# Optimization experiments

Measured on AMD Instinct MI355X. Metric: run time of the kernel, lower is better.

## Reference

```python
import jax, jax.numpy as jnp
import numpy as np

N_NODES = 100000
N_RADIAL = 16  # columns 0..15
N_CONICAL = 16  # columns 16..31


def setup_inputs() -> dict:
    key = jax.random.key(0)
    k1, k2, k3, k4 = jax.random.split(key, 4)
    x = jax.random.normal(k1, (N_NODES, 32), dtype=jnp.float32)
    edge_index = jax.random.randint(k2, (2, 1600000), 0, N_NODES, dtype=jnp.int32)
    W1 = jax.random.normal(k3, (32, 128), dtype=jnp.float32) * 0.1
    b1 = jnp.zeros((128,), dtype=jnp.float32)
    W2 = jax.random.normal(k4, (128, 32), dtype=jnp.float32) * 0.1
    b2 = jnp.zeros((32,), dtype=jnp.float32)
    return {"x": x, "edge_index": edge_index, "W1": W1, "b1": b1, "W2": W2, "b2": b2}


def reference(x, edge_index, W1, b1, W2, b2):
    # slice radial / conical feature channels
    radial = x[:, :N_RADIAL]            # [N, 16]
    conical = x[:, N_RADIAL:N_RADIAL + N_CONICAL]  # [N, 16]

    i, j = edge_index[0], edge_index[1]
    rows = jnp.concatenate([i, j])      # symmetrized COO rows [2E]
    cols = jnp.concatenate([j, i])      # symmetrized COO cols [2E]

    # coalesce()+sparse.mm == segment-sum over all (duplicated) entries
    neighbor_sum = jax.ops.segment_sum(conical[cols], rows, num_segments=N_NODES)  # [N, 16]
    deg = jax.ops.segment_sum(jnp.ones_like(rows, dtype=x.dtype), rows, num_segments=N_NODES)
    deg = jnp.clip(deg, 1.0)[:, None]   # bincount(...).clamp(min=1)
    agg = neighbor_sum / deg            # mean aggregation

    combined = jnp.concatenate([radial, agg], axis=1)  # [N, 32]
    h = jax.nn.relu(combined @ W1 + b1)
    out = h @ W2 + b2                   # [N, 32]
    return out
```

## Files before the change

kernel.cpp:

```cpp
#include <hip/hip_runtime.h>
#include <hip/hip_fp16.h>

#define N_NODES  100000
#define N_RADIAL 16
#define N_CONICAL 16

#define NPB    256
#define NBKT   ((N_NODES + NPB - 1) / NPB)
#define NBLK_A 500
#define BTHR   512
#define CHUNK  6400
#define BINSTRIDE 6400
#define CAP    10240

typedef _Float16 h2vec __attribute__((ext_vector_type(2)));
static __device__ __forceinline__ float fdot2(__half2 a, __half2 b, float c) {
    h2vec av, bv;
    __builtin_memcpy(&av, &a, 4);
    __builtin_memcpy(&bv, &b, 4);
    return __builtin_amdgcn_fdot2(av, bv, c, false);
}

__global__ __launch_bounds__(BTHR) void binfuse_kernel(
    const int* __restrict__ idx, const float* __restrict__ x,
    __half2* __restrict__ xcon2,
    const float* __restrict__ W1, const float* __restrict__ W2,
    float* __restrict__ W1tr, __half* __restrict__ W1th, __half* __restrict__ W2th,
    unsigned int* __restrict__ binned, int* __restrict__ cnts,
    int* __restrict__ offs, int total, int E) {
    int b = blockIdx.x, tid = threadIdx.x;
    if (b >= NBLK_A) {
        int pb = b - NBLK_A;
        if (pb == 0) {
            for (int i = tid; i < 2048; i += BTHR) {
                int k = i >> 4, c = i & 15;
                W1tr[k * 16 + c] = W1[c * 128 + k];
                W1th[k * 16 + c] = __float2half(W1[(16 + c) * 128 + k]);
            }
            for (int i = tid; i < 4096; i += BTHR) {
                int kk = i >> 5, o = i & 31;
                W2th[o * 128 + kk] = __float2half(W2[i]);
            }
        } else {
            int t = (pb - 1) * BTHR + tid;
            if (t < N_NODES * 4) {
                int n = t >> 2, p = t & 3;
                float4 v = *((const float4*)(x + (size_t)n * 32 + 16) + p);
                __half2 h0 = __floats2half2_rn(v.x, v.y);
                __half2 h1 = __floats2half2_rn(v.z, v.w);
                uint2 st;
                st.x = *(unsigned int*)&h0; st.y = *(unsigned int*)&h1;
                *(uint2*)(xcon2 + 2 * t) = st;
            }
        }
        return;
    }

    __shared__ int cnt[NBKT];
    __shared__ int loff[NBKT];
    __shared__ unsigned int stage[CHUNK];
    for (int i = tid; i < NBKT; i += BTHR) cnt[i] = 0;
    __syncthreads();

    int lo = b * CHUNK;
    int cofs = (lo >= E) ? -E : E;
    const int4* rp = (const int4*)(idx + lo);
    const int4* cp = (const int4*)(idx + lo + cofs);
    const int nq = CHUNK >> 2;

    int4 rr[4], cc[4];
    #pragma unroll
    for (int u = 0; u < 4; u++) {
        int q = tid + u * BTHR;
        if (q < nq) {
            rr[u] = rp[q];
            cc[u] = cp[q];
            atomicAdd(&cnt[rr[u].x >> 8], 1);
            atomicAdd(&cnt[rr[u].y >> 8], 1);
            atomicAdd(&cnt[rr[u].z >> 8], 1);
            atomicAdd(&cnt[rr[u].w >> 8], 1);
        }
    }
    __syncthreads();

    if (tid < 64) {
        int c[7]; int s = 0;
        #pragma unroll
        for (int u = 0; u < 7; u++) {
            int i = tid * 7 + u;
            c[u] = (i < NBKT) ? cnt[i] : 0;
            s += c[u];
        }
        int t = s;
        #pragma unroll
        for (int off = 1; off < 64; off <<= 1) {
            int u = __shfl_up(t, off, 64);
            if (tid >= off) t += u;
        }
        int ex = t - s;
        #pragma unroll
        for (int u = 0; u < 7; u++) {
            int i = tid * 7 + u;
            if (i < NBKT) { loff[i] = ex; ex += c[u]; }
        }
    }
    __syncthreads();

    for (int i = tid; i < NBKT; i += BTHR) {
        cnts[i * NBLK_A + b] = cnt[i];
        offs[i * NBLK_A + b] = loff[i];
    }
    __syncthreads();

    #pragma unroll
    for (int u = 0; u < 4; u++) {
        int q = tid + u * BTHR;
        if (q < nq) {
            int4 r = rr[u];
            int4 c = cc[u];
            int p0 = atomicAdd(&loff[r.x >> 8], 1);
            int p1 = atomicAdd(&loff[r.y >> 8], 1);
            int p2 = atomicAdd(&loff[r.z >> 8], 1);
            int p3 = atomicAdd(&loff[r.w >> 8], 1);
            stage[p0] = ((unsigned int)(r.x & 255) << 17) | (unsigned int)c.x;
            stage[p1] = ((unsigned int)(r.y & 255) << 17) | (unsigned int)c.y;
            stage[p2] = ((unsigned int)(r.z & 255) << 17) | (unsigned int)c.z;
            stage[p3] = ((unsigned int)(r.w & 255) << 17) | (unsigned int)c.w;
        }
    }
    __syncthreads();

    unsigned int* dst = binned + (size_t)b * BINSTRIDE;
    for (int i = tid; i < CHUNK; i += BTHR) dst[i] = stage[i];
}

__global__ __launch_bounds__(1024, 2) void agg_kernel(
    const __half* __restrict__ xcon, const int* __restrict__ cnts,
    const int* __restrict__ offs,
    const unsigned int* __restrict__ binned, __half* __restrict__ agg) {
    __shared__ unsigned int sedge[CAP];
    __shared__ int scnt[NPB];
    __shared__ int soff[NPB];
    int orig = blockIdx.x;
    int xcd = orig & 7, i8 = orig >> 3;
    const int qq = NBKT >> 3, rr = NBKT & 7;
    int b = (xcd < rr) ? xcd * (qq + 1) + i8
                       : rr * (qq + 1) + (xcd - rr) * qq + i8;
    int tid = threadIdx.x;
    if (tid < NPB) scnt[tid] = 0;
    __syncthreads();

    int sub = tid >> 1, l = tid & 1;
    int sc = 0; unsigned int base = 0;
    if (sub < NBLK_A) {
        sc   = cnts[b * NBLK_A + sub];
        base = (unsigned int)sub * BINSTRIDE
             + (unsigned int)offs[b * NBLK_A + sub];
    }
    int j0 = l ? (sc >> 1) : 0;
    int j1 = l ? sc : (sc >> 1);

    unsigned int ev[12];
    {
        const uint4* vp = (const uint4*)(binned + base + j0);
        uint4 v0 = vp[0], v1 = vp[1], v2 = vp[2];
        ev[0]=v0.x; ev[1]=v0.y; ev[2]=v0.z;  ev[3]=v0.w;
        ev[4]=v1.x; ev[5]=v1.y; ev[6]=v1.z;  ev[7]=v1.w;
        ev[8]=v2.x; ev[9]=v2.y; ev[10]=v2.z; ev[11]=v2.w;
    }
    #pragma unroll
    for (int u = 0; u < 12; u++)
        if (j0 + u < j1) atomicAdd(&scnt[ev[u] >> 17], 1);
    for (int j = j0 + 12; j < j1; j++)
        atomicAdd(&scnt[binned[base + j] >> 17], 1);
    __syncthreads();

    if (tid < 64) {
        int i0 = tid * 4;
        int c0 = scnt[i0], c1 = scnt[i0 + 1], c2 = scnt[i0 + 2], c3 = scnt[i0 + 3];
        int s = c0 + c1 + c2 + c3;
        int t = s;
        #pragma unroll
        for (int off = 1; off < 64; off <<= 1) {
            int u = __shfl_up(t, off, 64);
            if (tid >= off) t += u;
        }
        int ex = t - s;
        soff[i0]     = ex;
        soff[i0 + 1] = ex + c0;
        soff[i0 + 2] = ex + c0 + c1;
        soff[i0 + 3] = ex + c0 + c1 + c2;
    }
    __syncthreads();

    #pragma unroll
    for (int u = 0; u < 12; u++) {
        if (j0 + u < j1) {
            unsigned int p = ev[u];
            int pos = atomicAdd(&soff[p >> 17], 1);
            sedge[pos] = p & 0x1FFFFu;
        }
    }
    for (int j = j0 + 12; j < j1; j++) {
        unsigned int p = binned[base + j];
        int pos = atomicAdd(&soff[p >> 17], 1);
        sedge[pos] = p & 0x1FFFFu;
    }
    __syncthreads();

    if (tid < 2 * NPB) {
        int nl = tid >> 1, q = tid & 1;
        int c  = scnt[nl];
        int s0 = soff[nl] - c;
        float a0 = 0.f, a1 = 0.f, a2 = 0.f, a3 = 0.f;
        float a4 = 0.f, a5 = 0.f, a6 = 0.f, a7 = 0.f;
        #pragma unroll 2
        for (int k = 0; k < c; k++) {
            int col = (int)sedge[s0 + k];
            uint4 raw = ((const uint4*)(xcon + (size_t)col * 16))[q];
            float2 f0 = __half22float2(*(const __half2*)&raw.x);
            float2 f1 = __half22float2(*(const __half2*)&raw.y);
            float2 f2 = __half22float2(*(const __half2*)&raw.z);
            float2 f3 = __half22float2(*(const __half2*)&raw.w);
            a0 += f0.x; a1 += f0.y; a2 += f1.x; a3 += f1.y;
            a4 += f2.x; a5 += f2.y; a6 += f3.x; a7 += f3.y;
        }
        int n = b * NPB + nl;
        if (n < N_NODES) {
            float inv = 1.0f / (float)max(c, 1);
            __half2 h0 = __floats2half2_rn(a0 * inv, a1 * inv);
            __half2 h1 = __floats2half2_rn(a2 * inv, a3 * inv);
            __half2 h2 = __floats2half2_rn(a4 * inv, a5 * inv);
            __half2 h3 = __floats2half2_rn(a6 * inv, a7 * inv);
            uint4 st;
            st.x = *(unsigned int*)&h0; st.y = *(unsigned int*)&h1;
            st.z = *(unsigned int*)&h2; st.w = *(unsigned int*)&h3;
            *(uint4*)(agg + (size_t)n * 16 + q * 8) = st;
        }
    }
}

__global__ __launch_bounds__(512, 4) void mlp_kernel(
    const float* __restrict__ x, const __half* __restrict__ agg,
    const float* __restrict__ W1tr, const __half* __restrict__ W1th,
    const float* __restrict__ b1,
    const __half* __restrict__ W2th, const float* __restrict__ b2,
    float* __restrict__ out, int N) {
    __shared__ __half2 H2[64 * 64];
    int tid  = threadIdx.x;
    int lane = tid & 63;
    int ws   = __builtin_amdgcn_readfirstlane(tid >> 6);
    int n    = blockIdx.x * 64 + lane;
    int nc   = min(n, N - 1);

    float combr[16];
    const float4* xr = (const float4*)(x + (size_t)nc * 32);
    #pragma unroll
    for (int c = 0; c < 4; c++) {
        float4 v = xr[c];
        combr[c*4+0] = v.x; combr[c*4+1] = v.y;
        combr[c*4+2] = v.z; combr[c*4+3] = v.w;
    }
    __half2 aggh[8];
    const __half2* ar = (const __half2*)(agg + (size_t)nc * 16);
    #pragma unroll
    for (int c = 0; c < 8; c++) aggh[c] = ar[c];

    #pragma unroll
    for (int i = 0; i < 16; i += 2) {
        int k0 = ws * 16 + i;
        const float*   w1a  = W1tr + k0 * 16;
        const float*   w1b  = w1a + 16;
        const __half2* w1ha = (const __half2*)(W1th + k0 * 16);
        const __half2* w1hb = w1ha + 8;
        float ha = b1[k0], hb = b1[k0 + 1];
        #pragma unroll
        for (int c = 0; c < 16; c++) {
            ha = fmaf(combr[c], w1a[c], ha);
            hb = fmaf(combr[c], w1b[c], hb);
        }
        #pragma unroll
        for (int p = 0; p < 8; p++) {
            ha = fdot2(aggh[p], w1ha[p], ha);
            hb = fdot2(aggh[p], w1hb[p], hb);
        }
        ha = fmaxf(ha, 0.f); hb = fmaxf(hb, 0.f);
        H2[(k0 >> 1) * 64 + lane] = __floats2half2_rn(ha, hb);
    }
    __syncthreads();

    int o0 = ws * 4;
    const __half2* w20 = (const __half2*)(W2th + (o0 + 0) * 128);
    const __half2* w21 = (const __half2*)(W2th + (o0 + 1) * 128);
    const __half2* w22 = (const __half2*)(W2th + (o0 + 2) * 128);
    const __half2* w23 = (const __half2*)(W2th + (o0 + 3) * 128);
    float acc0 = b2[o0+0], acc1 = b2[o0+1], acc2 = b2[o0+2], acc3 = b2[o0+3];
    #pragma unroll 8
    for (int kp = 0; kp < 64; kp++) {
        __half2 hq = H2[kp * 64 + lane];
        acc0 = fdot2(hq, w20[kp], acc0);
        acc1 = fdot2(hq, w21[kp], acc1);
        acc2 = fdot2(hq, w22[kp], acc2);
        acc3 = fdot2(hq, w23[kp], acc3);
    }
    if (n < N) {
        float* op = out + (size_t)n * 32 + o0;
        op[0] = acc0; op[1] = acc1; op[2] = acc2; op[3] = acc3;
    }
}

extern "C" void kernel_launch(void* const* d_in, const int* in_sizes, int n_in,
                              void* d_out, int out_size, void* d_ws, size_t ws_size,
                              hipStream_t stream) {
    const float* x   = (const float*)d_in[0];
    const int*   idx = (const int*)d_in[1];
    const float* W1  = (const float*)d_in[2];
    const float* b1  = (const float*)d_in[3];
    const float* W2  = (const float*)d_in[4];
    const float* b2  = (const float*)d_in[5];
    float* out = (float*)d_out;

    const int E = in_sizes[1] / 2;
    const int total = 2 * E;

    char* base = (char*)d_ws;
    __half*       agg    = (__half*)base;
    __half*       xcon   = (__half*)(base + 3203072);
    float*        W1tr   = (float*)(base + 6406144);
    __half*       W1th   = (__half*)(base + 6414336);
    __half*       W2th   = (__half*)(base + 6418432);
    int*          cnts   = (int*)(base + 6426624);
    int*          offs   = (int*)(base + 7208960);
    unsigned int* binned = (unsigned int*)(base + 7991296);

    int pack_blocks = (N_NODES * 4 + BTHR - 1) / BTHR;
    binfuse_kernel<<<NBLK_A + 1 + pack_blocks, BTHR, 0, stream>>>(
        idx, x, (__half2*)xcon, W1, W2, W1tr, W1th, W2th,
        binned, cnts, offs, total, E);
    agg_kernel<<<NBKT, 1024, 0, stream>>>(xcon, cnts, offs, binned, agg);
    mlp_kernel<<<(N_NODES + 63) / 64, 512, 0, stream>>>(
        x, agg, W1tr, W1th, b1, W2th, b2, out, N_NODES);
}
```

Baseline: 133.5 us.

## Compute per-node degree with global atomics during binning; accumulate in fp16

The binning kernel now also runs a global atomicAdd per edge row into a per-node degree array, which is cleared with a memset. The aggregation kernel then reads those degrees to build its local counts and prefix offsets directly, removing one pass of shared-memory atomics and a barrier. Neighbor sums are also accumulated as packed half2 adds instead of being converted to fp32 first. In exchange this adds 3.2M scattered global atomics, an extra memset launch, and a risk of fp16 accumulation error or overflow on high-degree nodes.

```diff
diff --git a/kernel.cpp b/kernel.cpp
--- a/kernel.cpp
+++ b/kernel.cpp
@@ -12,6 +12,7 @@
 #define CHUNK  6400
 #define BINSTRIDE 6400
 #define CAP    10240
+#define NDEG   100096
 
 typedef _Float16 h2vec __attribute__((ext_vector_type(2)));
 static __device__ __forceinline__ float fdot2(__half2 a, __half2 b, float c) {
@@ -27,7 +28,7 @@
     const float* __restrict__ W1, const float* __restrict__ W2,
     float* __restrict__ W1tr, __half* __restrict__ W1th, __half* __restrict__ W2th,
     unsigned int* __restrict__ binned, int* __restrict__ cnts,
-    int* __restrict__ offs, int total, int E) {
+    int* __restrict__ offs, int* __restrict__ deg, int total, int E) {
     int b = blockIdx.x, tid = threadIdx.x;
     if (b >= NBLK_A) {
         int pb = b - NBLK_A;
@@ -79,6 +80,10 @@
             atomicAdd(&cnt[rr[u].y >> 8], 1);
             atomicAdd(&cnt[rr[u].z >> 8], 1);
             atomicAdd(&cnt[rr[u].w >> 8], 1);
+            atomicAdd(&deg[rr[u].x], 1);
+            atomicAdd(&deg[rr[u].y], 1);
+            atomicAdd(&deg[rr[u].z], 1);
+            atomicAdd(&deg[rr[u].w], 1);
         }
     }
     __syncthreads();
@@ -137,7 +142,8 @@
 __global__ __launch_bounds__(1024, 2) void agg_kernel(
     const __half* __restrict__ xcon, const int* __restrict__ cnts,
     const int* __restrict__ offs,
-    const unsigned int* __restrict__ binned, __half* __restrict__ agg) {
+    const unsigned int* __restrict__ binned,
+    const int* __restrict__ deg, __half* __restrict__ agg) {
     __shared__ unsigned int sedge[CAP];
     __shared__ int scnt[NPB];
     __shared__ int soff[NPB];
@@ -147,7 +153,27 @@
     int b = (xcd < rr) ? xcd * (qq + 1) + i8
                        : rr * (qq + 1) + (xcd - rr) * qq + i8;
     int tid = threadIdx.x;
-    if (tid < NPB) scnt[tid] = 0;
+
+    if (tid < 64) {
+        int i0 = tid * 4;
+        int4 d4 = *(const int4*)(deg + b * NPB + i0);
+        scnt[i0]     = d4.x;
+        scnt[i0 + 1] = d4.y;
+        scnt[i0 + 2] = d4.z;
+        scnt[i0 + 3] = d4.w;
+        int s = d4.x + d4.y + d4.z + d4.w;
+        int t = s;
+        #pragma unroll
+        for (int off = 1; off < 64; off <<= 1) {
+            int u = __shfl_up(t, off, 64);
+            if (tid >= off) t += u;
+        }
+        int ex = t - s;
+        soff[i0]     = ex;
+        soff[i0 + 1] = ex + d4.x;
+        soff[i0 + 2] = ex + d4.x + d4.y;
+        soff[i0 + 3] = ex + d4.x + d4.y + d4.z;
+    }
     __syncthreads();
 
     int sub = tid >> 1, l = tid & 1;
@@ -169,31 +195,6 @@
         ev[8]=v2.x; ev[9]=v2.y; ev[10]=v2.z; ev[11]=v2.w;
     }
     #pragma unroll
-    for (int u = 0; u < 12; u++)
-        if (j0 + u < j1) atomicAdd(&scnt[ev[u] >> 17], 1);
-    for (int j = j0 + 12; j < j1; j++)
-        atomicAdd(&scnt[binned[base + j] >> 17], 1);
-    __syncthreads();
-
-    if (tid < 64) {
-        int i0 = tid * 4;
-        int c0 = scnt[i0], c1 = scnt[i0 + 1], c2 = scnt[i0 + 2], c3 = scnt[i0 + 3];
-        int s = c0 + c1 + c2 + c3;
-        int t = s;
-        #pragma unroll
-        for (int off = 1; off < 64; off <<= 1) {
-            int u = __shfl_up(t, off, 64);
-            if (tid >= off) t += u;
-        }
-        int ex = t - s;
-        soff[i0]     = ex;
-        soff[i0 + 1] = ex + c0;
-        soff[i0 + 2] = ex + c0 + c1;
-        soff[i0 + 3] = ex + c0 + c1 + c2;
-    }
-    __syncthreads();
-
-    #pragma unroll
     for (int u = 0; u < 12; u++) {
         if (j0 + u < j1) {
             unsigned int p = ev[u];
@@ -212,26 +213,28 @@
         int nl = tid >> 1, q = tid & 1;
         int c  = scnt[nl];
         int s0 = soff[nl] - c;
-        float a0 = 0.f, a1 = 0.f, a2 = 0.f, a3 = 0.f;
-        float a4 = 0.f, a5 = 0.f, a6 = 0.f, a7 = 0.f;
+        __half2 z = __floats2half2_rn(0.f, 0.f);
+        __half2 ah0 = z, ah1 = z, ah2 = z, ah3 = z;
         #pragma unroll 2
         for (int k = 0; k < c; k++) {
             int col = (int)sedge[s0 + k];
             uint4 raw = ((const uint4*)(xcon + (size_t)col * 16))[q];
-            float2 f0 = __half22float2(*(const __half2*)&raw.x);
-            float2 f1 = __half22float2(*(const __half2*)&raw.y);
-            float2 f2 = __half22float2(*(const __half2*)&raw.z);
-            float2 f3 = __half22float2(*(const __half2*)&raw.w);
-            a0 += f0.x; a1 += f0.y; a2 += f1.x; a3 += f1.y;
-            a4 += f2.x; a5 += f2.y; a6 += f3.x; a7 += f3.y;
+            ah0 = __hadd2(ah0, *(const __half2*)&raw.x);
+            ah1 = __hadd2(ah1, *(const __half2*)&raw.y);
+            ah2 = __hadd2(ah2, *(const __half2*)&raw.z);
+            ah3 = __hadd2(ah3, *(const __half2*)&raw.w);
         }
         int n = b * NPB + nl;
         if (n < N_NODES) {
             float inv = 1.0f / (float)max(c, 1);
-            __half2 h0 = __floats2half2_rn(a0 * inv, a1 * inv);
-            __half2 h1 = __floats2half2_rn(a2 * inv, a3 * inv);
-            __half2 h2 = __floats2half2_rn(a4 * inv, a5 * inv);
-            __half2 h3 = __floats2half2_rn(a6 * inv, a7 * inv);
+            float2 f0 = __half22float2(ah0);
+            float2 f1 = __half22float2(ah1);
+            float2 f2 = __half22float2(ah2);
+            float2 f3 = __half22float2(ah3);
+            __half2 h0 = __floats2half2_rn(f0.x * inv, f0.y * inv);
+            __half2 h1 = __floats2half2_rn(f1.x * inv, f1.y * inv);
+            __half2 h2 = __floats2half2_rn(f2.x * inv, f2.y * inv);
+            __half2 h3 = __floats2half2_rn(f3.x * inv, f3.y * inv);
             uint4 st;
             st.x = *(unsigned int*)&h0; st.y = *(unsigned int*)&h1;
             st.z = *(unsigned int*)&h2; st.w = *(unsigned int*)&h3;
@@ -329,15 +332,18 @@
     float*        W1tr   = (float*)(base + 6406144);
     __half*       W1th   = (__half*)(base + 6414336);
     __half*       W2th   = (__half*)(base + 6418432);
-    int*          cnts   = (int*)(base + 6426624);
-    int*          offs   = (int*)(base + 7208960);
-    unsigned int* binned = (unsigned int*)(base + 7991296);
+    int*          deg    = (int*)(base + 6426624);
+    int*          cnts   = (int*)(base + 6827008);
+    int*          offs   = (int*)(base + 7609344);
+    unsigned int* binned = (unsigned int*)(base + 8391680);
+
+    hipMemsetAsync(deg, 0, NDEG * sizeof(int), stream);
 
     int pack_blocks = (N_NODES * 4 + BTHR - 1) / BTHR;
     binfuse_kernel<<<NBLK_A + 1 + pack_blocks, BTHR, 0, stream>>>(
         idx, x, (__half2*)xcon, W1, W2, W1tr, W1th, W2th,
-        binned, cnts, offs, total, E);
-    agg_kernel<<<NBKT, 1024, 0, stream>>>(xcon, cnts, offs, binned, agg);
+        binned, cnts, offs, deg, total, E);
+    agg_kernel<<<NBKT, 1024, 0, stream>>>(xcon, cnts, offs, binned, deg, agg);
     mlp_kernel<<<(N_NODES + 63) / 64, 512, 0, stream>>>(
         x, agg, W1tr, W1th, b1, W2th, b2, out, N_NODES);
 }
```

Result: slower. 255.2 us (+91.2%).
